# Performance work log

Hardware: AMD Instinct MI355X
Metric: run time of the kernel (lower is better)

The kernel has to match this reference:

```python
import jax, jax.numpy as jnp
import numpy as np

N, M, E, HID, H = 50000, 4000, 320000, 128, 2
EPS = 1e-5  # torch BatchNorm1d eps


def _lrelu(x):
    return jnp.where(x >= 0, x, 0.2 * x)


def _bn(x, g, b):
    # BatchNorm1d in training mode: biased batch statistics over dim 0
    m = x.mean(0)
    v = ((x - m) ** 2).mean(0)
    return g * (x - m) * jax.lax.rsqrt(v + EPS) + b


def _seg_softmax(a, idx, n):
    # softmax of a[E,heads] normalized per node index idx (PyG softmax)
    mx = jax.ops.segment_max(a, idx, num_segments=n)
    e = jnp.exp(a - mx[idx])
    s = jax.ops.segment_sum(e, idx, num_segments=n)
    return e / s[idx]


def _hgconv(x, he_n, he_e, he_w, W, att, bias, heads):
    # PyG HypergraphConv(use_attention=True, concat=False)
    xl = (x @ W).reshape(N, heads, HID)                  # lin(x) -> [N,heads,C]
    # hyperedge_attr = incidence^T @ x  (matches to_dense_adj path in HGAT)
    ea = jax.ops.segment_sum(x[he_n], he_e, num_segments=M)  # [M,F]
    eal = (ea @ W).reshape(M, heads, HID)                # lin(hyperedge_attr)
    a = (jnp.concatenate([xl[he_n], eal[he_e]], axis=-1) * att[0]).sum(-1)  # [E,heads]
    a = _seg_softmax(_lrelu(a), he_n, N)
    # degree normalizations
    Dn = jax.ops.segment_sum(he_w[he_e], he_n, num_segments=N)
    Dinv = jnp.where(Dn > 0, 1.0 / Dn, 0.0)
    Bn = jax.ops.segment_sum(jnp.ones((E,), x.dtype), he_e, num_segments=M)
    Binv = jnp.where(Bn > 0, 1.0 / Bn, 0.0)
    # node -> hyperedge
    m1 = Binv[he_e][:, None, None] * xl[he_n] * a[..., None]
    eo = jax.ops.segment_sum(m1, he_e, num_segments=M)   # [M,heads,C]
    # hyperedge -> node
    m2 = Dinv[he_n][:, None, None] * eo[he_e] * a[..., None]
    out = jax.ops.segment_sum(m2, he_n, num_segments=N)  # [N,heads,C]
    return out.mean(1) + bias                            # concat=False -> head mean


def _forward(x, he_w, lin1_w, lin1_b, bn1_g, bn1_b, h1_w, h1_att, h1_b,
             bn2_g, bn2_b, h2_w, h2_att, h2_b, bn3_g, bn3_b,
             lin2_w, lin2_b, bn4_g, bn4_b, he_n, he_e):
    src = x
    x = _bn(_lrelu(x @ lin1_w + lin1_b), bn1_g, bn1_b)
    x2 = _hgconv(x, he_n, he_e, he_w, h1_w, h1_att, h1_b, H)
    x = _bn(x + x2, bn2_g, bn2_b)
    x2 = _hgconv(x, he_n, he_e, he_w, h2_w, h2_att, h2_b, 1)
    x = _bn(x + x2, bn3_g, bn3_b)
    x = _lrelu(x @ lin2_w + lin2_b)
    return _bn(src + x, bn4_g, bn4_b)


def setup_inputs() -> dict:
    key = jax.random.key(0)
    ks = jax.random.split(key, 10)
    s = 0.05
    he_n = jax.random.randint(ks[0], (E,), 0, N, dtype=jnp.int32)
    he_e = (jnp.arange(E, dtype=jnp.int32) % M)  # every hyperedge id used
    return {
        'x': jax.random.normal(ks[1], (N, 128), jnp.float32),
        'he_n': he_n, 'he_e': he_e,
        'he_w': jnp.ones((M,), jnp.float32),
        'lin1_w': jax.random.normal(ks[2], (128, HID), jnp.float32) * s,
        'lin1_b': jnp.zeros((HID,), jnp.float32),
        'bn1_g': jnp.ones((HID,), jnp.float32), 'bn1_b': jnp.zeros((HID,), jnp.float32),
        'h1_w': jax.random.normal(ks[3], (HID, H * HID), jnp.float32) * s,
        'h1_att': jax.random.normal(ks[4], (1, H, 2 * HID), jnp.float32) * s,
        'h1_b': jnp.zeros((HID,), jnp.float32),
        'bn2_g': jnp.ones((HID,), jnp.float32), 'bn2_b': jnp.zeros((HID,), jnp.float32),
        'h2_w': jax.random.normal(ks[5], (HID, HID), jnp.float32) * s,
        'h2_att': jax.random.normal(ks[6], (1, 1, 2 * HID), jnp.float32) * s,
        'h2_b': jnp.zeros((HID,), jnp.float32),
        'bn3_g': jnp.ones((HID,), jnp.float32), 'bn3_b': jnp.zeros((HID,), jnp.float32),
        'lin2_w': jax.random.normal(ks[7], (HID, 128), jnp.float32) * s,
        'lin2_b': jnp.zeros((128,), jnp.float32),
        'bn4_g': jnp.ones((128,), jnp.float32), 'bn4_b': jnp.zeros((128,), jnp.float32),
    }


def reference(x, he_n, he_e, he_w, lin1_w, lin1_b, bn1_g, bn1_b, h1_w, h1_att, h1_b,
              bn2_g, bn2_b, h2_w, h2_att, h2_b, bn3_g, bn3_b,
              lin2_w, lin2_b, bn4_g, bn4_b):
    return _forward(x, he_w, lin1_w, lin1_b, bn1_g, bn1_b, h1_w, h1_att, h1_b,
                    bn2_g, bn2_b, h2_w, h2_att, h2_b, bn3_g, bn3_b,
                    lin2_w, lin2_b, bn4_g, bn4_b, he_n, he_e)
```

## Files before the change

### kernel.cpp

```cpp
#include <hip/hip_runtime.h>
#include <math.h>

constexpr int Nn = 50000;
constexpr int Mm = 4000;
constexpr int Ee = 320000;
constexpr int KPB = Ee / Mm;
constexpr float BINV = 1.0f / (float)KPB;
constexpr float EPSf = 1e-5f;
constexpr int NBKT = 16;
constexpr int NBSCAN = 49;

__device__ __forceinline__ float lrelu_f(float x) { return x >= 0.f ? x : 0.2f * x; }

__device__ __forceinline__ float wave_sum(float v) {
#pragma unroll
    for (int o = 32; o >= 1; o >>= 1) v += __shfl_xor(v, o, 64);
    return v;
}

__device__ __forceinline__ void finalize_to_lds(const float* __restrict__ st,
                                                const float* __restrict__ g,
                                                const float* __restrict__ b,
                                                float* ABsh, int t) {
    if (t < 128) {
        double ds = 0, dq = 0;
#pragma unroll
        for (int i = 0; i < NBKT; i++) {
            ds += (double)st[i * 256 + t];
            dq += (double)st[i * 256 + 128 + t];
        }
        double mean = ds / (double)Nn;
        double var = dq / (double)Nn - mean * mean;
        float rstd = (float)(1.0 / sqrt(var + (double)EPSf));
        float A = g[t] * rstd;
        ABsh[t] = A;
        ABsh[128 + t] = b[t] - (float)mean * A;
    }
    __syncthreads();
}

__device__ void scan_body(const int* __restrict__ counts, int* __restrict__ offs,
                          int b, int t) {
    __shared__ int sdi[256];
    int pre = 0;
    for (int i = t; i < b * 1024; i += 256) pre += counts[i];
    sdi[t] = pre;
    __syncthreads();
    for (int st = 128; st >= 1; st >>= 1) {
        if (t < st) sdi[t] += sdi[t + st];
        __syncthreads();
    }
    int run0 = sdi[0];
    __syncthreads();
    int c4[4];
    int s = 0;
#pragma unroll
    for (int i = 0; i < 4; i++) {
        int n = b * 1024 + t * 4 + i;
        c4[i] = (n < Nn) ? counts[n] : 0;
        s += c4[i];
    }
    sdi[t] = s;
    __syncthreads();
    for (int off = 1; off < 256; off <<= 1) {
        int v = (t >= off) ? sdi[t - off] : 0;
        __syncthreads();
        sdi[t] += v;
        __syncthreads();
    }
    int run = sdi[t] - s + run0;
#pragma unroll
    for (int i = 0; i < 4; i++) {
        int n = b * 1024 + t * 4 + i;
        if (n < Nn) offs[n] = run;
        run += c4[i];
    }
    if (b == NBSCAN - 1 && t == 255) offs[Nn] = run0 + sdi[255];
}

template <int ROWS, bool LRELU, bool PROBN, bool RESID, bool STATS, bool PACKH2, bool SCANX>
__global__ __launch_bounds__(256) void gemmT(const float* __restrict__ A, size_t aystride,
                                             const float* __restrict__ B, int ldb,
                                             const float* __restrict__ bias, float scale,
                                             const float* __restrict__ stIn,
                                             const float* __restrict__ fing,
                                             const float* __restrict__ finb,
                                             const float* __restrict__ resid,
                                             float* __restrict__ stF,
                                             float* __restrict__ C, int ldc, int R,
                                             int gemmBlocksX,
                                             const int* __restrict__ counts,
                                             int* __restrict__ offs) {
    constexpr int RPT = ROWS / 16;
    const int t = threadIdx.x;
    if (SCANX && (int)blockIdx.x >= gemmBlocksX) {
        if (blockIdx.y == 0) scan_body(counts, offs, blockIdx.x - gemmBlocksX, t);
        return;
    }
    __shared__ float As[16][ROWS + 4];
    __shared__ float Bs[16][128];
    __shared__ float Sred[STATS ? 16 : 1][STATS ? 128 : 1];
    __shared__ float ABsh[PROBN ? 256 : 1];
    const int ty = t >> 4, tx = t & 15;
    const int row0 = blockIdx.x * ROWS;
    const int bcol = blockIdx.y * 128;
    A += (size_t)blockIdx.y * aystride;

    if (PROBN) finalize_to_lds(stIn, fing, finb, ABsh, t);

    float4 acc[RPT][2];
#pragma unroll
    for (int i = 0; i < RPT; i++)
#pragma unroll
        for (int q = 0; q < 2; q++) acc[i][q] = make_float4(0.f, 0.f, 0.f, 0.f);

    for (int k0 = 0; k0 < 128; k0 += 16) {
        if (ROWS == 64) {
            int r = t >> 2, kc = (t & 3) * 4;
            int rr = row0 + r;
            rr = rr < R ? rr : R - 1;
            float4 av = *(const float4*)(A + (size_t)rr * 128 + k0 + kc);
            if (PROBN) {
                float4 sA = *(const float4*)&ABsh[k0 + kc];
                float4 sB = *(const float4*)&ABsh[128 + k0 + kc];
                av.x = av.x * sA.x + sB.x; av.y = av.y * sA.y + sB.y;
                av.z = av.z * sA.z + sB.z; av.w = av.w * sA.w + sB.w;
            }
            As[kc + 0][r] = av.x; As[kc + 1][r] = av.y;
            As[kc + 2][r] = av.z; As[kc + 3][r] = av.w;
        } else {
            int r = t >> 3, kc = (t & 7) * 2;
            int rr = row0 + r;
            rr = rr < R ? rr : R - 1;
            float2 av = *(const float2*)(A + (size_t)rr * 128 + k0 + kc);
            if (PROBN) {
                av.x = av.x * ABsh[k0 + kc] + ABsh[128 + k0 + kc];
                av.y = av.y * ABsh[k0 + kc + 1] + ABsh[128 + k0 + kc + 1];
            }
            As[kc + 0][r] = av.x;
            As[kc + 1][r] = av.y;
        }
        {
            int kk = t >> 5, c4 = (t & 31) * 4;
            float4 bv0 = *(const float4*)(B + (size_t)(k0 + kk) * ldb + bcol + c4);
            float4 bv1 = *(const float4*)(B + (size_t)(k0 + kk + 8) * ldb + bcol + c4);
            *(float4*)&Bs[kk][c4] = bv0;
            *(float4*)&Bs[kk + 8][c4] = bv1;
        }
        __syncthreads();
#pragma unroll
        for (int kk = 0; kk < 16; kk++) {
            float ar[RPT];
            if (RPT == 4) {
                float4 a4 = *(const float4*)&As[kk][ty * 4];
                ar[0] = a4.x; ar[1] = a4.y; ar[2] = a4.z; ar[3] = a4.w;
            } else {
                float2 a2 = *(const float2*)&As[kk][ty * 2];
                ar[0] = a2.x; ar[RPT - 1] = a2.y;
            }
            float4 b0 = *(const float4*)&Bs[kk][4 * tx];
            float4 b1 = *(const float4*)&Bs[kk][64 + 4 * tx];
#pragma unroll
            for (int i = 0; i < RPT; i++) {
                acc[i][0].x = fmaf(ar[i], b0.x, acc[i][0].x);
                acc[i][0].y = fmaf(ar[i], b0.y, acc[i][0].y);
                acc[i][0].z = fmaf(ar[i], b0.z, acc[i][0].z);
                acc[i][0].w = fmaf(ar[i], b0.w, acc[i][0].w);
                acc[i][1].x = fmaf(ar[i], b1.x, acc[i][1].x);
                acc[i][1].y = fmaf(ar[i], b1.y, acc[i][1].y);
                acc[i][1].z = fmaf(ar[i], b1.z, acc[i][1].z);
                acc[i][1].w = fmaf(ar[i], b1.w, acc[i][1].w);
            }
        }
        __syncthreads();
    }

    float4 bv0 = make_float4(0.f, 0.f, 0.f, 0.f), bv1 = bv0;
    if (bias) {
        bv0 = *(const float4*)(bias + bcol + 4 * tx);
        bv1 = *(const float4*)(bias + bcol + 64 + 4 * tx);
    }
    float4 cs0 = make_float4(0.f, 0.f, 0.f, 0.f), cs1 = cs0, cq0 = cs0, cq1 = cs0;
#pragma unroll
    for (int i = 0; i < RPT; i++) {
        int row = row0 + ty * RPT + i;
        if (row >= R) continue;
        float4 v0, v1;
        v0.x = acc[i][0].x * scale + bv0.x; v0.y = acc[i][0].y * scale + bv0.y;
        v0.z = acc[i][0].z * scale + bv0.z; v0.w = acc[i][0].w * scale + bv0.w;
        v1.x = acc[i][1].x * scale + bv1.x; v1.y = acc[i][1].y * scale + bv1.y;
        v1.z = acc[i][1].z * scale + bv1.z; v1.w = acc[i][1].w * scale + bv1.w;
        if (LRELU) {
            v0.x = lrelu_f(v0.x); v0.y = lrelu_f(v0.y); v0.z = lrelu_f(v0.z); v0.w = lrelu_f(v0.w);
            v1.x = lrelu_f(v1.x); v1.y = lrelu_f(v1.y); v1.z = lrelu_f(v1.z); v1.w = lrelu_f(v1.w);
        }
        if (RESID) {
            float4 r0 = *(const float4*)(resid + (size_t)row * 128 + bcol + 4 * tx);
            float4 r1 = *(const float4*)(resid + (size_t)row * 128 + bcol + 64 + 4 * tx);
            v0.x += r0.x; v0.y += r0.y; v0.z += r0.z; v0.w += r0.w;
            v1.x += r1.x; v1.y += r1.y; v1.z += r1.z; v1.w += r1.w;
        }
        if (PACKH2) {
            int h = blockIdx.y;
            float* c0 = C + (size_t)row * ldc + 8 * tx + 2 * h;
            *(float2*)(c0) = make_float2(v0.x, v0.y);
            *(float2*)(c0 + 4) = make_float2(v0.z, v0.w);
            float* c1 = C + (size_t)row * ldc + 128 + 8 * tx + 2 * h;
            *(float2*)(c1) = make_float2(v1.x, v1.y);
            *(float2*)(c1 + 4) = make_float2(v1.z, v1.w);
        } else {
            *(float4*)(C + (size_t)row * ldc + bcol + 4 * tx) = v0;
            *(float4*)(C + (size_t)row * ldc + bcol + 64 + 4 * tx) = v1;
        }
        if (STATS) {
            cs0.x += v0.x; cs0.y += v0.y; cs0.z += v0.z; cs0.w += v0.w;
            cs1.x += v1.x; cs1.y += v1.y; cs1.z += v1.z; cs1.w += v1.w;
            cq0.x += v0.x * v0.x; cq0.y += v0.y * v0.y; cq0.z += v0.z * v0.z; cq0.w += v0.w * v0.w;
            cq1.x += v1.x * v1.x; cq1.y += v1.y * v1.y; cq1.z += v1.z * v1.z; cq1.w += v1.w * v1.w;
        }
    }
    if (STATS) {
        int bkt = blockIdx.x & (NBKT - 1);
#pragma unroll
        for (int pass = 0; pass < 2; pass++) {
            *(float4*)&Sred[ty][4 * tx] = pass ? cq0 : cs0;
            *(float4*)&Sred[ty][64 + 4 * tx] = pass ? cq1 : cs1;
            __syncthreads();
            if (t < 128) {
                float tot = 0.f;
#pragma unroll
                for (int r = 0; r < 16; r++) tot += Sred[r][t];
                atomicAdd(&stF[bkt * 256 + pass * 128 + t], tot);
            }
            __syncthreads();
        }
    }
}

__global__ void count_edges_watt(const int* __restrict__ he_n, int* __restrict__ counts,
                                 const float* __restrict__ h1_w, const float* __restrict__ h1_att,
                                 const float* __restrict__ h2_w, const float* __restrict__ h2_att,
                                 float* __restrict__ wnA, float* __restrict__ weA,
                                 int* __restrict__ he_nT) {
    int t = threadIdx.x;
    if (blockIdx.x == 1250) {
        for (int j = 0; j < 3; j++) {
            int id = t + 256 * j;
            if (id >= 768) break;
            int which = id / 384;
            int rem = id % 384;
            int h3 = rem >> 7, k = rem & 127;
            float s = 0.f;
            if (h3 < 2) {
                const float* wrow = h1_w + (size_t)k * 256 + h3 * 128;
                const float* arow = h1_att + h3 * 256 + which * 128;
                for (int c = 0; c < 128; c++) s += wrow[c] * arow[c];
            } else {
                const float* wrow = h2_w + (size_t)k * 128;
                const float* arow = h2_att + which * 128;
                for (int c = 0; c < 128; c++) s += wrow[c] * arow[c];
            }
            (which ? weA : wnA)[h3 * 128 + k] = s;
        }
        return;
    }
    int g = blockIdx.x * 256 + t;
    if (g < Ee) {
        int m = g / KPB;
        int k = g - m * KPB;
        int n = he_n[m + (size_t)k * Mm];
        he_nT[g] = n;
        atomicAdd(&counts[n], 1);
    }
}

template <int H, bool FILL>
__global__ __launch_bounds__(256) void bn_dots(const float* __restrict__ X,
                                               const float* __restrict__ stIn,
                                               const float* __restrict__ fing,
                                               const float* __restrict__ finb,
                                               float* __restrict__ ABout,
                                               const float* __restrict__ wn,
                                               const float* __restrict__ we,
                                               float* __restrict__ an,
                                               float* __restrict__ pe,
                                               const int* __restrict__ he_n,
                                               const int* __restrict__ offs,
                                               int* __restrict__ cursor,
                                               int* __restrict__ eid, int mainBlocks) {
    int t = threadIdx.x;
    if (FILL && (int)blockIdx.x >= mainBlocks) {
        int e = (blockIdx.x - mainBlocks) * 256 + t;
        if (e < Ee) {
            int n = he_n[e];
            int p = atomicAdd(&cursor[n], 1);
            eid[offs[n] + p] = e;
        }
        return;
    }
    __shared__ float ABsh[256];
    finalize_to_lds(stIn, fing, finb, ABsh, t);
    if (blockIdx.x == 0) ABout[t] = ABsh[t];
    int w = t >> 6, lane = t & 63;
    float a0 = ABsh[lane], a1 = ABsh[lane + 64];
    float b0 = ABsh[128 + lane], b1 = ABsh[192 + lane];
    float wn0[H], wn1[H], we0[H], we1[H];
#pragma unroll
    for (int h = 0; h < H; h++) {
        wn0[h] = wn[h * 128 + lane]; wn1[h] = wn[h * 128 + 64 + lane];
        we0[h] = we[h * 128 + lane]; we1[h] = we[h * 128 + 64 + lane];
    }
#pragma unroll
    for (int nn = 0; nn < 4; nn++) {
        int row = blockIdx.x * 16 + w * 4 + nn;
        const float* xr = X + (size_t)row * 128;
        float v0 = xr[lane] * a0 + b0;
        float v1 = xr[lane + 64] * a1 + b1;
        float pv[H], qv[H];
#pragma unroll
        for (int h = 0; h < H; h++) {
            pv[h] = wave_sum(v0 * wn0[h] + v1 * wn1[h]);
            qv[h] = wave_sum(v0 * we0[h] + v1 * we1[h]);
        }
        if (lane == 0) {
            if (H == 2) {
                *(float2*)&an[row * 2] = make_float2(pv[0], pv[1]);
                *(float2*)&pe[row * 2] = make_float2(qv[0], qv[1]);
            } else {
                an[row] = pv[0];
                pe[row] = qv[0];
            }
        }
    }
}

__global__ __launch_bounds__(256) void bn_out(const float* __restrict__ X,
                                              const float* __restrict__ stIn,
                                              const float* __restrict__ fing,
                                              const float* __restrict__ finb,
                                              float* __restrict__ Y) {
    __shared__ float ABsh[256];
    int t = threadIdx.x;
    finalize_to_lds(stIn, fing, finb, ABsh, t);
    int w = t >> 6, lane = t & 63;
    float a0 = ABsh[lane], a1 = ABsh[lane + 64];
    float b0 = ABsh[128 + lane], b1 = ABsh[192 + lane];
#pragma unroll
    for (int nn = 0; nn < 4; nn++) {
        int row = blockIdx.x * 16 + w * 4 + nn;
        const float* xr = X + (size_t)row * 128;
        float* yr = Y + (size_t)row * 128;
        yr[lane] = xr[lane] * a0 + b0;
        yr[lane + 64] = xr[lane + 64] * a1 + b1;
    }
}

template <int H>
__global__ __launch_bounds__(256) void ea_from_pe(const int* __restrict__ he_nT,
                                                  const float* __restrict__ pe,
                                                  float* __restrict__ ae) {
    int w = threadIdx.x >> 6, lane = threadIdx.x & 63;
    int m = blockIdx.x * 4 + w;
    if (m >= Mm) return;
    float s[H];
#pragma unroll
    for (int h = 0; h < H; h++) s[h] = 0.f;
    for (int k = lane; k < KPB; k += 64) {
        int idx = he_nT[m * KPB + k];
        if (H == 2) {
            float2 p2 = *(const float2*)(pe + (size_t)idx * 2);
            s[0] += p2.x;
            s[H - 1] += p2.y;
        } else {
            s[0] += pe[idx];
        }
    }
#pragma unroll
    for (int h = 0; h < H; h++) s[h] = wave_sum(s[h]);
    if (lane == 0)
#pragma unroll
        for (int h = 0; h < H; h++) ae[m * H + h] = s[h];
}

template <int H>
__global__ __launch_bounds__(256) void seg_softmax(const int* __restrict__ offs,
                                                   const int* __restrict__ eid,
                                                   const float* __restrict__ an,
                                                   const float* __restrict__ ae,
                                                   const float* __restrict__ he_w,
                                                   float* __restrict__ nsp) {
    int t = threadIdx.x;
    int wv = t >> 6, lane = t & 63;
    int q = lane >> 3, li = lane & 7;
    int n = blockIdx.x * 32 + wv * 8 + q;
    bool valid = n < Nn;
    int base = valid ? offs[n] : 0;
    int deg = valid ? offs[n + 1] - base : 0;
    float anv[H];
#pragma unroll
    for (int h = 0; h < H; h++) anv[h] = valid ? an[n * H + h] : 0.f;

    bool h0 = li < deg, h1 = li + 8 < deg;
    int m0 = 0, m1 = 0;
    float l0[H], l1[H];
    float mx[H];
#pragma unroll
    for (int h = 0; h < H; h++) { mx[h] = -INFINITY; l0[h] = 0.f; l1[h] = 0.f; }
    if (h0) {
        m0 = eid[base + li] % Mm;
#pragma unroll
        for (int h = 0; h < H; h++) {
            l0[h] = lrelu_f(anv[h] + ae[m0 * H + h]);
            mx[h] = fmaxf(mx[h], l0[h]);
        }
    }
    if (h1) {
        m1 = eid[base + li + 8] % Mm;
#pragma unroll
        for (int h = 0; h < H; h++) {
            l1[h] = lrelu_f(anv[h] + ae[m1 * H + h]);
            mx[h] = fmaxf(mx[h], l1[h]);
        }
    }
    for (int c = li + 16; c < deg; c += 8) {
        int m = eid[base + c] % Mm;
#pragma unroll
        for (int h = 0; h < H; h++) mx[h] = fmaxf(mx[h], lrelu_f(anv[h] + ae[m * H + h]));
    }
#pragma unroll
    for (int h = 0; h < H; h++) {
#pragma unroll
        for (int o = 1; o <= 4; o <<= 1) mx[h] = fmaxf(mx[h], __shfl_xor(mx[h], o, 64));
    }
    float sm[H];
#pragma unroll
    for (int h = 0; h < H; h++) sm[h] = 0.f;
    float dn = 0.f;
    if (h0) {
        dn += he_w[m0];
#pragma unroll
        for (int h = 0; h < H; h++) sm[h] += expf(l0[h] - mx[h]);
    }
    if (h1) {
        dn += he_w[m1];
#pragma unroll
        for (int h = 0; h < H; h++) sm[h] += expf(l1[h] - mx[h]);
    }
    for (int c = li + 16; c < deg; c += 8) {
        int m = eid[base + c] % Mm;
        dn += he_w[m];
#pragma unroll
        for (int h = 0; h < H; h++) sm[h] += expf(lrelu_f(anv[h] + ae[m * H + h]) - mx[h]);
    }
#pragma unroll
    for (int o = 1; o <= 4; o <<= 1) dn += __shfl_xor(dn, o, 64);
#pragma unroll
    for (int h = 0; h < H; h++) {
#pragma unroll
        for (int o = 1; o <= 4; o <<= 1) sm[h] += __shfl_xor(sm[h], o, 64);
    }
    if (valid && li == 0) {
        float Dv = dn > 0.f ? 1.0f / dn : 0.0f;
        if (H == 2) {
            *(float4*)(nsp + (size_t)n * 8) = make_float4(anv[0], anv[H - 1], mx[0], mx[H - 1]);
            *(float4*)(nsp + (size_t)n * 8 + 4) =
                make_float4(1.f / sm[0], 1.f / sm[H - 1], 0.5f * Dv, 0.f);
        } else {
            *(float4*)(nsp + (size_t)n * 4) = make_float4(anv[0], mx[0], 1.f / sm[0], Dv);
        }
    }
}

template <int H>
__global__ __launch_bounds__(256) void s_build(const float* __restrict__ X,
                                               const float* __restrict__ AB,
                                               const int* __restrict__ he_nT,
                                               const float* __restrict__ nsp,
                                               const float* __restrict__ ae,
                                               float* __restrict__ S) {
    __shared__ int idx[KPB];
    __shared__ float av[KPB][H];
    __shared__ float red[8][H][128];
    int m = blockIdx.x, t = threadIdx.x;
    int g = t >> 5, l = t & 31;
    if (t < KPB) {
        int nd = he_nT[m * KPB + t];
        idx[t] = nd;
        if (H == 2) {
            float4 pa = *(const float4*)(nsp + (size_t)nd * 8);
            float4 pb = *(const float4*)(nsp + (size_t)nd * 8 + 4);
            float2 a2 = *(const float2*)(ae + (size_t)m * 2);
            av[t][0] = expf(lrelu_f(pa.x + a2.x) - pa.z) * pb.x;
            av[t][H - 1] = expf(lrelu_f(pa.y + a2.y) - pa.w) * pb.y;
        } else {
            float4 pa = *(const float4*)(nsp + (size_t)nd * 4);
            float aem = ae[m];
            av[t][0] = expf(lrelu_f(pa.x + aem) - pa.y) * pa.z;
        }
    }
    __syncthreads();
    float4 A4 = ((const float4*)AB)[l];
    float4 B4 = ((const float4*)(AB + 128))[l];
    float4 acc[H];
#pragma unroll
    for (int h = 0; h < H; h++) acc[h] = make_float4(0.f, 0.f, 0.f, 0.f);
#pragma unroll
    for (int kk = 0; kk < KPB / 8; kk++) {
        int k = g + kk * 8;
        float4 v = ((const float4*)(X + (size_t)idx[k] * 128))[l];
        v.x = v.x * A4.x + B4.x;
        v.y = v.y * A4.y + B4.y;
        v.z = v.z * A4.z + B4.z;
        v.w = v.w * A4.w + B4.w;
#pragma unroll
        for (int h = 0; h < H; h++) {
            float a = av[k][h];
            acc[h].x = fmaf(a, v.x, acc[h].x);
            acc[h].y = fmaf(a, v.y, acc[h].y);
            acc[h].z = fmaf(a, v.z, acc[h].z);
            acc[h].w = fmaf(a, v.w, acc[h].w);
        }
    }
#pragma unroll
    for (int h = 0; h < H; h++) *(float4*)&red[g][h][l * 4] = acc[h];
    __syncthreads();
    if (t < 32 * H) {
        int h = t >> 5, l2 = t & 31;
        float4 s = make_float4(0.f, 0.f, 0.f, 0.f);
#pragma unroll
        for (int gg = 0; gg < 8; gg++) {
            float4 r = *(const float4*)&red[gg][h][l2 * 4];
            s.x += r.x; s.y += r.y; s.z += r.z; s.w += r.w;
        }
        ((float4*)(S + ((size_t)h * Mm + m) * 128))[l2] = s;
    }
}

template <int H>
__global__ __launch_bounds__(256) void node_agg(const int* __restrict__ offs,
                                                const int* __restrict__ eid,
                                                const float* __restrict__ nsp,
                                                const float* __restrict__ ae,
                                                const float* __restrict__ eo,
                                                const float* __restrict__ bias,
                                                const float* __restrict__ AB,
                                                float* __restrict__ stF,
                                                float* __restrict__ T) {
    __shared__ float smem[4][256];
    __shared__ float redS[4][128], redQ[4][128];
    int t = threadIdx.x;
    int w = t >> 6, lane = t & 63;
    int n0 = blockIdx.x * 16 + w * 4;
    int o = offs[n0 + (lane < 4 ? lane : 4)];
    int b0 = __shfl(o, 0, 64);
    int b1 = __shfl(o, 1, 64);
    int b2 = __shfl(o, 2, 64);
    int b3 = __shfl(o, 3, 64);
    int b4 = __shfl(o, 4, 64);
    int cnt = b4 - b0;
    int cnt64 = cnt < 64 ? cnt : 64;

    if (lane < cnt64) {
        int slot = b0 + lane;
        int j = (slot >= b1) + (slot >= b2) + (slot >= b3);
        int e = eid[slot];
        int m = e % Mm;
        if (H == 2) {
            float4 pa = *(const float4*)(nsp + (size_t)(n0 + j) * 8);
            float4 pb = *(const float4*)(nsp + (size_t)(n0 + j) * 8 + 4);
            float2 a2 = *(const float2*)(ae + (size_t)m * 2);
            float c0 = expf(lrelu_f(pa.x + a2.x) - pa.z) * pb.x * pb.z;
            float c1 = expf(lrelu_f(pa.y + a2.y) - pa.w) * pb.y * pb.z;
            *(float4*)&smem[w][4 * lane] = make_float4(__int_as_float(m), c0, c1, 0.f);
        } else {
            float4 pa = *(const float4*)(nsp + (size_t)(n0 + j) * 4);
            float c = expf(lrelu_f(pa.x + ae[m]) - pa.y) * pa.z * pa.w;
            *(float2*)&smem[w][2 * lane] = make_float2(__int_as_float(m), c);
        }
    }
    __syncthreads();

    int s1 = min(b1 - b0, cnt64), s2 = min(b2 - b0, cnt64), s3 = min(b3 - b0, cnt64);
    float2 acc0 = make_float2(0.f, 0.f), acc1 = acc0, acc2 = acc0, acc3 = acc0;

#define NA_BODY(ACC, CBEG, CEND)                                                \
    {                                                                           \
        int c = (CBEG);                                                         \
        for (; c + 1 < (CEND); c += 2) {                                        \
            if (H == 2) {                                                       \
                float4 sa = *(const float4*)&smem[w][4 * c];                    \
                float4 sb = *(const float4*)&smem[w][4 * (c + 1)];              \
                float4 ea = *(const float4*)(eo + (size_t)__float_as_int(sa.x) * 256 + 4 * lane); \
                float4 eb = *(const float4*)(eo + (size_t)__float_as_int(sb.x) * 256 + 4 * lane); \
                ACC.x += sa.y * ea.x + sa.z * ea.z + sb.y * eb.x + sb.z * eb.z; \
                ACC.y += sa.y * ea.y + sa.z * ea.w + sb.y * eb.y + sb.z * eb.w; \
            } else {                                                            \
                float2 sa = *(const float2*)&smem[w][2 * c];                    \
                float2 sb = *(const float2*)&smem[w][2 * (c + 1)];              \
                float2 ea = *(const float2*)(eo + (size_t)__float_as_int(sa.x) * 128 + 2 * lane); \
                float2 eb = *(const float2*)(eo + (size_t)__float_as_int(sb.x) * 128 + 2 * lane); \
                ACC.x += sa.y * ea.x + sb.y * eb.x;                             \
                ACC.y += sa.y * ea.y + sb.y * eb.y;                             \
            }                                                                   \
        }                                                                       \
        if (c < (CEND)) {                                                       \
            if (H == 2) {                                                       \
                float4 sa = *(const float4*)&smem[w][4 * c];                    \
                float4 ea = *(const float4*)(eo + (size_t)__float_as_int(sa.x) * 256 + 4 * lane); \
                ACC.x += sa.y * ea.x + sa.z * ea.z;                             \
                ACC.y += sa.y * ea.y + sa.z * ea.w;                             \
            } else {                                                            \
                float2 sa = *(const float2*)&smem[w][2 * c];                    \
                float2 ea = *(const float2*)(eo + (size_t)__float_as_int(sa.x) * 128 + 2 * lane); \
                ACC.x += sa.y * ea.x;                                           \
                ACC.y += sa.y * ea.y;                                           \
            }                                                                   \
        }                                                                       \
    }
    NA_BODY(acc0, 0, s1)
    NA_BODY(acc1, s1, s2)
    NA_BODY(acc2, s2, s3)
    NA_BODY(acc3, s3, cnt64)
#undef NA_BODY

    for (int ss = 64; ss < cnt; ss++) {
        int slot = b0 + ss;
        int j = (slot >= b1) + (slot >= b2) + (slot >= b3);
        int e = eid[slot];
        int m = e % Mm;
        float cx, cy;
        if (H == 2) {
            float4 pa = *(const float4*)(nsp + (size_t)(n0 + j) * 8);
            float4 pb = *(const float4*)(nsp + (size_t)(n0 + j) * 8 + 4);
            float2 a2 = *(const float2*)(ae + (size_t)m * 2);
            float c0 = expf(lrelu_f(pa.x + a2.x) - pa.z) * pb.x * pb.z;
            float c1 = expf(lrelu_f(pa.y + a2.y) - pa.w) * pb.y * pb.z;
            float4 ev = *(const float4*)(eo + (size_t)m * 256 + 4 * lane);
            cx = c0 * ev.x + c1 * ev.z;
            cy = c0 * ev.y + c1 * ev.w;
        } else {
            float4 pa = *(const float4*)(nsp + (size_t)(n0 + j) * 4);
            float c = expf(lrelu_f(pa.x + ae[m]) - pa.y) * pa.z * pa.w;
            float2 ev = *(const float2*)(eo + (size_t)m * 128 + 2 * lane);
            cx = c * ev.x;
            cy = c * ev.y;
        }
        if (j == 0) { acc0.x += cx; acc0.y += cy; }
        else if (j == 1) { acc1.x += cx; acc1.y += cy; }
        else if (j == 2) { acc2.x += cx; acc2.y += cy; }
        else { acc3.x += cx; acc3.y += cy; }
    }

    int col = 2 * lane;
    float2 A2 = *(const float2*)(AB + col);
    float2 B2 = *(const float2*)(AB + 128 + col);
    float2 bi = *(const float2*)(bias + col);
    float cs0 = 0.f, cs1 = 0.f, cq0 = 0.f, cq1 = 0.f;
    float2 accs[4] = {acc0, acc1, acc2, acc3};
#pragma unroll
    for (int j = 0; j < 4; j++) {
        int n = n0 + j;
        float2 xr = *(const float2*)(T + (size_t)n * 128 + col);
        float r0 = xr.x * A2.x + B2.x + bi.x + accs[j].x;
        float r1 = xr.y * A2.y + B2.y + bi.y + accs[j].y;
        *(float2*)(T + (size_t)n * 128 + col) = make_float2(r0, r1);
        cs0 += r0; cs1 += r1;
        cq0 += r0 * r0; cq1 += r1 * r1;
    }
    redS[w][col] = cs0; redS[w][col + 1] = cs1;
    redQ[w][col] = cq0; redQ[w][col + 1] = cq1;
    __syncthreads();
    if (t < 128) {
        float s = 0.f, qq = 0.f;
#pragma unroll
        for (int ww = 0; ww < 4; ww++) { s += redS[ww][t]; qq += redQ[ww][t]; }
        int bkt = blockIdx.x & (NBKT - 1);
        atomicAdd(&stF[bkt * 256 + t], s);
        atomicAdd(&stF[bkt * 256 + 128 + t], qq);
    }
}

extern "C" void kernel_launch(void* const* d_in, const int* in_sizes, int n_in,
                              void* d_out, int out_size, void* d_ws, size_t ws_size,
                              hipStream_t stream) {
    const float* x = (const float*)d_in[0];
    const int* he_n = (const int*)d_in[1];
    const float* he_w = (const float*)d_in[3];
    const float* lin1_w = (const float*)d_in[4];
    const float* lin1_b = (const float*)d_in[5];
    const float* bn1_g = (const float*)d_in[6];
    const float* bn1_b = (const float*)d_in[7];
    const float* h1_w = (const float*)d_in[8];
    const float* h1_att = (const float*)d_in[9];
    const float* h1_b = (const float*)d_in[10];
    const float* bn2_g = (const float*)d_in[11];
    const float* bn2_b = (const float*)d_in[12];
    const float* h2_w = (const float*)d_in[13];
    const float* h2_att = (const float*)d_in[14];
    const float* h2_b = (const float*)d_in[15];
    const float* bn3_g = (const float*)d_in[16];
    const float* bn3_b = (const float*)d_in[17];
    const float* lin2_w = (const float*)d_in[18];
    const float* lin2_b = (const float*)d_in[19];
    const float* bn4_g = (const float*)d_in[20];
    const float* bn4_b = (const float*)d_in[21];
    float* out = (float*)d_out;

    char* ws = (char*)d_ws;
    size_t off = 0;
    auto alloc = [&](size_t bytes) -> char* {
        char* p = ws + off;
        off = (off + bytes + 255) & ~(size_t)255;
        return p;
    };
    int* counts = (int*)alloc((size_t)Nn * 4);
    int* cursor = (int*)alloc((size_t)Nn * 4);
    float* stats = (float*)alloc((size_t)4 * NBKT * 256 * 4);
    size_t zbytes = off;
    int* offs = (int*)alloc((size_t)(Nn + 1) * 4);
    int* eid = (int*)alloc((size_t)Ee * 4);
    int* he_nT = (int*)alloc((size_t)Ee * 4);
    float* an = (float*)alloc((size_t)Nn * 2 * 4);
    float* pe = (float*)alloc((size_t)Nn * 2 * 4);
    float* ae = (float*)alloc((size_t)Mm * 2 * 4);
    float* nsp = (float*)alloc((size_t)Nn * 8 * 4);
    float* S = (float*)alloc((size_t)2 * Mm * 128 * 4);
    float* eo = (float*)alloc((size_t)2 * Mm * 128 * 4);
    float* wnA = (float*)alloc(384 * 4);
    float* weA = (float*)alloc(384 * 4);
    float* AB = (float*)alloc(2 * 256 * 4);
    float* buf = (float*)alloc((size_t)Nn * 128 * 4);

    float* st0 = stats;
    float* st1 = stats + NBKT * 256;
    float* st2 = stats + 2 * NBKT * 256;
    float* st3 = stats + 3 * NBKT * 256;
    float *AB1 = AB, *AB2 = AB + 256;

    hipMemsetAsync(d_ws, 0, zbytes, stream);

    constexpr int GB32 = (Nn + 31) / 32;
    count_edges_watt<<<1251, 256, 0, stream>>>(he_n, counts, h1_w, h1_att, h2_w, h2_att,
                                               wnA, weA, he_nT);

    gemmT<32, true, false, false, true, false, true><<<dim3(GB32 + NBSCAN, 1), 256, 0, stream>>>(
        x, 0, lin1_w, 128, lin1_b, 1.f, nullptr, nullptr, nullptr, nullptr, st0, buf, 128, Nn,
        GB32, counts, offs);
    bn_dots<2, true><<<3125 + 1250, 256, 0, stream>>>(buf, st0, bn1_g, bn1_b, AB1, wnA, weA,
                                                      an, pe, he_n, offs, cursor, eid, 3125);

    ea_from_pe<2><<<Mm / 4, 256, 0, stream>>>(he_nT, pe, ae);
    seg_softmax<2><<<(Nn + 31) / 32, 256, 0, stream>>>(offs, eid, an, ae, he_w, nsp);
    s_build<2><<<Mm, 256, 0, stream>>>(buf, AB1, he_nT, nsp, ae, S);
    gemmT<32, false, false, false, false, true, false><<<dim3(125, 2), 256, 0, stream>>>(
        S, (size_t)Mm * 128, h1_w, 256, nullptr, BINV, nullptr, nullptr, nullptr, nullptr,
        nullptr, eo, 256, Mm, 125, nullptr, nullptr);
    node_agg<2><<<3125, 256, 0, stream>>>(offs, eid, nsp, ae, eo, h1_b, AB1, st1, buf);

    bn_dots<1, false><<<3125, 256, 0, stream>>>(buf, st1, bn2_g, bn2_b, AB2, wnA + 256,
                                                weA + 256, an, pe, nullptr, nullptr, nullptr,
                                                nullptr, 3125);

    ea_from_pe<1><<<Mm / 4, 256, 0, stream>>>(he_nT, pe, ae);
    seg_softmax<1><<<(Nn + 31) / 32, 256, 0, stream>>>(offs, eid, an, ae, he_w, nsp);
    s_build<1><<<Mm, 256, 0, stream>>>(buf, AB2, he_nT, nsp, ae, S);
    gemmT<32, false, false, false, false, false, false><<<dim3(125, 1), 256, 0, stream>>>(
        S, 0, h2_w, 128, nullptr, BINV, nullptr, nullptr, nullptr, nullptr, nullptr,
        eo, 128, Mm, 125, nullptr, nullptr);
    node_agg<1><<<3125, 256, 0, stream>>>(offs, eid, nsp, ae, eo, h2_b, AB2, st2, buf);

    gemmT<32, true, true, true, true, false, false><<<dim3(GB32, 1), 256, 0, stream>>>(
        buf, 0, lin2_w, 128, lin2_b, 1.f, st2, bn3_g, bn3_b, x, st3, buf, 128, Nn,
        GB32, nullptr, nullptr);
    bn_out<<<3125, 256, 0, stream>>>(buf, st3, bn4_g, bn4_b, out);
}
```

Before: 394.0 us.

## Add single-stage full-K GEMM kernel for node-level linear layers

Adds a gemmB kernel for the two N-row linear layers. It loads the whole 128x128 weight matrix and a 32x128 A tile into one 80KB LDS pool, then runs the full K loop with no per-k-slice barriers. The existing gemmT is reduced to the plain variant used by the hyperedge GEMMs. This removes the 8 load/sync rounds per block, but the large LDS footprint limits blocks per CU, so latency hiding drops and every block must reload the full weight matrix.

Result: slower. 417.3 us (+5.9%).

```diff
diff --git a/kernel.cpp b/kernel.cpp
--- a/kernel.cpp
+++ b/kernel.cpp
@@ -40,8 +40,7 @@
 }
 
 __device__ void scan_body(const int* __restrict__ counts, int* __restrict__ offs,
-                          int b, int t) {
-    __shared__ int sdi[256];
+                          int b, int t, int* sdi) {
     int pre = 0;
     for (int i = t; i < b * 1024; i += 256) pre += counts[i];
     sdi[t] = pre;
@@ -78,36 +77,159 @@
     if (b == NBSCAN - 1 && t == 255) offs[Nn] = run0 + sdi[255];
 }
 
-template <int ROWS, bool LRELU, bool PROBN, bool RESID, bool STATS, bool PACKH2, bool SCANX>
-__global__ __launch_bounds__(256) void gemmT(const float* __restrict__ A, size_t aystride,
-                                             const float* __restrict__ B, int ldb,
-                                             const float* __restrict__ bias, float scale,
+template <bool LRELU, bool PROBN, bool RESID, bool STATS, bool SCANX>
+__global__ __launch_bounds__(256) void gemmB(const float* __restrict__ A,
+                                             const float* __restrict__ B,
+                                             const float* __restrict__ bias,
                                              const float* __restrict__ stIn,
                                              const float* __restrict__ fing,
                                              const float* __restrict__ finb,
                                              const float* __restrict__ resid,
                                              float* __restrict__ stF,
-                                             float* __restrict__ C, int ldc, int R,
+                                             float* __restrict__ C, int R,
                                              int gemmBlocksX,
                                              const int* __restrict__ counts,
                                              int* __restrict__ offs) {
+    __shared__ float pool[20480];
+    const int t = threadIdx.x;
+    if (SCANX && (int)blockIdx.x >= gemmBlocksX) {
+        scan_body(counts, offs, blockIdx.x - gemmBlocksX, t, (int*)pool);
+        return;
+    }
+    const int ty = t >> 4, tx = t & 15;
+    const int row0 = blockIdx.x * 32;
+    const int rA = t & 31, kA = (t >> 5) * 16;
+
+    float Areg[16], Breg[16];
+    if (PROBN) {
+        finalize_to_lds(stIn, fing, finb, pool, t);
+#pragma unroll
+        for (int j = 0; j < 16; j++) {
+            Areg[j] = pool[kA + j];
+            Breg[j] = pool[128 + kA + j];
+        }
+        __syncthreads();
+    }
+
+    {
+        const int cB = (t & 31) * 4, kB0 = (t >> 5) * 16;
+#pragma unroll
+        for (int j = 0; j < 16; j++) {
+            float4 bv = *(const float4*)(B + (size_t)(kB0 + j) * 128 + cB);
+            *(float4*)&pool[4096 + (kB0 + j) * 128 + cB] = bv;
+        }
+    }
+    {
+        int rr = row0 + rA;
+        rr = rr < R ? rr : R - 1;
+        const float* Ar = A + (size_t)rr * 128 + kA;
+#pragma unroll
+        for (int p = 0; p < 4; p++) {
+            float4 av = *(const float4*)(Ar + 4 * p);
+            float vv[4] = {av.x, av.y, av.z, av.w};
+#pragma unroll
+            for (int q = 0; q < 4; q++) {
+                float v = vv[q];
+                if (PROBN) v = v * Areg[4 * p + q] + Breg[4 * p + q];
+                pool[(kA + 4 * p + q) * 32 + rA] = v;
+            }
+        }
+    }
+    __syncthreads();
+
+    float4 acc[2][2];
+#pragma unroll
+    for (int i = 0; i < 2; i++)
+#pragma unroll
+        for (int q = 0; q < 2; q++) acc[i][q] = make_float4(0.f, 0.f, 0.f, 0.f);
+
+#pragma unroll 8
+    for (int kk = 0; kk < 128; kk++) {
+        float2 a2 = *(const float2*)&pool[kk * 32 + ty * 2];
+        float4 b0 = *(const float4*)&pool[4096 + kk * 128 + 4 * tx];
+        float4 b1 = *(const float4*)&pool[4096 + kk * 128 + 64 + 4 * tx];
+        float ar[2] = {a2.x, a2.y};
+#pragma unroll
+        for (int i = 0; i < 2; i++) {
+            acc[i][0].x = fmaf(ar[i], b0.x, acc[i][0].x);
+            acc[i][0].y = fmaf(ar[i], b0.y, acc[i][0].y);
+            acc[i][0].z = fmaf(ar[i], b0.z, acc[i][0].z);
+            acc[i][0].w = fmaf(ar[i], b0.w, acc[i][0].w);
+            acc[i][1].x = fmaf(ar[i], b1.x, acc[i][1].x);
+            acc[i][1].y = fmaf(ar[i], b1.y, acc[i][1].y);
+            acc[i][1].z = fmaf(ar[i], b1.z, acc[i][1].z);
+            acc[i][1].w = fmaf(ar[i], b1.w, acc[i][1].w);
+        }
+    }
+
+    float4 bv0 = make_float4(0.f, 0.f, 0.f, 0.f), bv1 = bv0;
+    if (bias) {
+        bv0 = *(const float4*)(bias + 4 * tx);
+        bv1 = *(const float4*)(bias + 64 + 4 * tx);
+    }
+    float4 cs0 = make_float4(0.f, 0.f, 0.f, 0.f), cs1 = cs0, cq0 = cs0, cq1 = cs0;
+#pragma unroll
+    for (int i = 0; i < 2; i++) {
+        int row = row0 + ty * 2 + i;
+        if (row >= R) continue;
+        float4 v0, v1;
+        v0.x = acc[i][0].x + bv0.x; v0.y = acc[i][0].y + bv0.y;
+        v0.z = acc[i][0].z + bv0.z; v0.w = acc[i][0].w + bv0.w;
+        v1.x = acc[i][1].x + bv1.x; v1.y = acc[i][1].y + bv1.y;
+        v1.z = acc[i][1].z + bv1.z; v1.w = acc[i][1].w + bv1.w;
+        if (LRELU) {
+            v0.x = lrelu_f(v0.x); v0.y = lrelu_f(v0.y); v0.z = lrelu_f(v0.z); v0.w = lrelu_f(v0.w);
+            v1.x = lrelu_f(v1.x); v1.y = lrelu_f(v1.y); v1.z = lrelu_f(v1.z); v1.w = lrelu_f(v1.w);
+        }
+        if (RESID) {
+            float4 r0 = *(const float4*)(resid + (size_t)row * 128 + 4 * tx);
+            float4 r1 = *(const float4*)(resid + (size_t)row * 128 + 64 + 4 * tx);
+            v0.x += r0.x; v0.y += r0.y; v0.z += r0.z; v0.w += r0.w;
+            v1.x += r1.x; v1.y += r1.y; v1.z += r1.z; v1.w += r1.w;
+        }
+        *(float4*)(C + (size_t)row * 128 + 4 * tx) = v0;
+        *(float4*)(C + (size_t)row * 128 + 64 + 4 * tx) = v1;
+        if (STATS) {
+            cs0.x += v0.x; cs0.y += v0.y; cs0.z += v0.z; cs0.w += v0.w;
+            cs1.x += v1.x; cs1.y += v1.y; cs1.z += v1.z; cs1.w += v1.w;
+            cq0.x += v0.x * v0.x; cq0.y += v0.y * v0.y; cq0.z += v0.z * v0.z; cq0.w += v0.w * v0.w;
+            cq1.x += v1.x * v1.x; cq1.y += v1.y * v1.y; cq1.z += v1.z * v1.z; cq1.w += v1.w * v1.w;
+        }
+    }
+    if (STATS) {
+        __syncthreads();
+        float (*Sred)[128] = (float(*)[128])pool;
+        int bkt = blockIdx.x & (NBKT - 1);
+#pragma unroll
+        for (int pass = 0; pass < 2; pass++) {
+            *(float4*)&Sred[ty][4 * tx] = pass ? cq0 : cs0;
+            *(float4*)&Sred[ty][64 + 4 * tx] = pass ? cq1 : cs1;
+            __syncthreads();
+            if (t < 128) {
+                float tot = 0.f;
+#pragma unroll
+                for (int r = 0; r < 16; r++) tot += Sred[r][t];
+                atomicAdd(&stF[bkt * 256 + pass * 128 + t], tot);
+            }
+            __syncthreads();
+        }
+    }
+}
+
+template <int ROWS, bool PACKH2>
+__global__ __launch_bounds__(256) void gemmT(const float* __restrict__ A, size_t aystride,
+                                             const float* __restrict__ B, int ldb,
+                                             float scale,
+                                             float* __restrict__ C, int ldc, int R) {
     constexpr int RPT = ROWS / 16;
     const int t = threadIdx.x;
-    if (SCANX && (int)blockIdx.x >= gemmBlocksX) {
-        if (blockIdx.y == 0) scan_body(counts, offs, blockIdx.x - gemmBlocksX, t);
-        return;
-    }
     __shared__ float As[16][ROWS + 4];
     __shared__ float Bs[16][128];
-    __shared__ float Sred[STATS ? 16 : 1][STATS ? 128 : 1];
-    __shared__ float ABsh[PROBN ? 256 : 1];
     const int ty = t >> 4, tx = t & 15;
     const int row0 = blockIdx.x * ROWS;
     const int bcol = blockIdx.y * 128;
     A += (size_t)blockIdx.y * aystride;
 
-    if (PROBN) finalize_to_lds(stIn, fing, finb, ABsh, t);
-
     float4 acc[RPT][2];
 #pragma unroll
     for (int i = 0; i < RPT; i++)
@@ -115,28 +237,11 @@
         for (int q = 0; q < 2; q++) acc[i][q] = make_float4(0.f, 0.f, 0.f, 0.f);
 
     for (int k0 = 0; k0 < 128; k0 += 16) {
-        if (ROWS == 64) {
-            int r = t >> 2, kc = (t & 3) * 4;
-            int rr = row0 + r;
-            rr = rr < R ? rr : R - 1;
-            float4 av = *(const float4*)(A + (size_t)rr * 128 + k0 + kc);
-            if (PROBN) {
-                float4 sA = *(const float4*)&ABsh[k0 + kc];
-                float4 sB = *(const float4*)&ABsh[128 + k0 + kc];
-                av.x = av.x * sA.x + sB.x; av.y = av.y * sA.y + sB.y;
-                av.z = av.z * sA.z + sB.z; av.w = av.w * sA.w + sB.w;
-            }
-            As[kc + 0][r] = av.x; As[kc + 1][r] = av.y;
-            As[kc + 2][r] = av.z; As[kc + 3][r] = av.w;
-        } else {
+        {
             int r = t >> 3, kc = (t & 7) * 2;
             int rr = row0 + r;
             rr = rr < R ? rr : R - 1;
             float2 av = *(const float2*)(A + (size_t)rr * 128 + k0 + kc);
-            if (PROBN) {
-                av.x = av.x * ABsh[k0 + kc] + ABsh[128 + k0 + kc];
-                av.y = av.y * ABsh[k0 + kc + 1] + ABsh[128 + k0 + kc + 1];
-            }
             As[kc + 0][r] = av.x;
             As[kc + 1][r] = av.y;
         }
@@ -151,10 +256,7 @@
 #pragma unroll
         for (int kk = 0; kk < 16; kk++) {
             float ar[RPT];
-            if (RPT == 4) {
-                float4 a4 = *(const float4*)&As[kk][ty * 4];
-                ar[0] = a4.x; ar[1] = a4.y; ar[2] = a4.z; ar[3] = a4.w;
-            } else {
+            {
                 float2 a2 = *(const float2*)&As[kk][ty * 2];
                 ar[0] = a2.x; ar[RPT - 1] = a2.y;
             }
@@ -175,31 +277,15 @@
         __syncthreads();
     }
 
-    float4 bv0 = make_float4(0.f, 0.f, 0.f, 0.f), bv1 = bv0;
-    if (bias) {
-        bv0 = *(const float4*)(bias + bcol + 4 * tx);
-        bv1 = *(const float4*)(bias + bcol + 64 + 4 * tx);
-    }
-    float4 cs0 = make_float4(0.f, 0.f, 0.f, 0.f), cs1 = cs0, cq0 = cs0, cq1 = cs0;
 #pragma unroll
     for (int i = 0; i < RPT; i++) {
         int row = row0 + ty * RPT + i;
         if (row >= R) continue;
         float4 v0, v1;
-        v0.x = acc[i][0].x * scale + bv0.x; v0.y = acc[i][0].y * scale + bv0.y;
-        v0.z = acc[i][0].z * scale + bv0.z; v0.w = acc[i][0].w * scale + bv0.w;
-        v1.x = acc[i][1].x * scale + bv1.x; v1.y = acc[i][1].y * scale + bv1.y;
-        v1.z = acc[i][1].z * scale + bv1.z; v1.w = acc[i][1].w * scale + bv1.w;
-        if (LRELU) {
-            v0.x = lrelu_f(v0.x); v0.y = lrelu_f(v0.y); v0.z = lrelu_f(v0.z); v0.w = lrelu_f(v0.w);
-            v1.x = lrelu_f(v1.x); v1.y = lrelu_f(v1.y); v1.z = lrelu_f(v1.z); v1.w = lrelu_f(v1.w);
-        }
-        if (RESID) {
-            float4 r0 = *(const float4*)(resid + (size_t)row * 128 + bcol + 4 * tx);
-            float4 r1 = *(const float4*)(resid + (size_t)row * 128 + bcol + 64 + 4 * tx);
-            v0.x += r0.x; v0.y += r0.y; v0.z += r0.z; v0.w += r0.w;
-            v1.x += r1.x; v1.y += r1.y; v1.z += r1.z; v1.w += r1.w;
-        }
+        v0.x = acc[i][0].x * scale; v0.y = acc[i][0].y * scale;
+        v0.z = acc[i][0].z * scale; v0.w = acc[i][0].w * scale;
+        v1.x = acc[i][1].x * scale; v1.y = acc[i][1].y * scale;
+        v1.z = acc[i][1].z * scale; v1.w = acc[i][1].w * scale;
         if (PACKH2) {
             int h = blockIdx.y;
             float* c0 = C + (size_t)row * ldc + 8 * tx + 2 * h;
@@ -211,28 +297,6 @@
         } else {
             *(float4*)(C + (size_t)row * ldc + bcol + 4 * tx) = v0;
             *(float4*)(C + (size_t)row * ldc + bcol + 64 + 4 * tx) = v1;
-        }
-        if (STATS) {
-            cs0.x += v0.x; cs0.y += v0.y; cs0.z += v0.z; cs0.w += v0.w;
-            cs1.x += v1.x; cs1.y += v1.y; cs1.z += v1.z; cs1.w += v1.w;
-            cq0.x += v0.x * v0.x; cq0.y += v0.y * v0.y; cq0.z += v0.z * v0.z; cq0.w += v0.w * v0.w;
-            cq1.x += v1.x * v1.x; cq1.y += v1.y * v1.y; cq1.z += v1.z * v1.z; cq1.w += v1.w * v1.w;
-        }
-    }
-    if (STATS) {
-        int bkt = blockIdx.x & (NBKT - 1);
-#pragma unroll
-        for (int pass = 0; pass < 2; pass++) {
-            *(float4*)&Sred[ty][4 * tx] = pass ? cq0 : cs0;
-            *(float4*)&Sred[ty][64 + 4 * tx] = pass ? cq1 : cs1;
-            __syncthreads();
-            if (t < 128) {
-                float tot = 0.f;
-#pragma unroll
-                for (int r = 0; r < 16; r++) tot += Sred[r][t];
-                atomicAdd(&stF[bkt * 256 + pass * 128 + t], tot);
-            }
-            __syncthreads();
         }
     }
 }
@@ -743,8 +807,8 @@
     count_edges_watt<<<1251, 256, 0, stream>>>(he_n, counts, h1_w, h1_att, h2_w, h2_att,
                                                wnA, weA, he_nT);
 
-    gemmT<32, true, false, false, true, false, true><<<dim3(GB32 + NBSCAN, 1), 256, 0, stream>>>(
-        x, 0, lin1_w, 128, lin1_b, 1.f, nullptr, nullptr, nullptr, nullptr, st0, buf, 128, Nn,
+    gemmB<true, false, false, true, true><<<GB32 + NBSCAN, 256, 0, stream>>>(
+        x, lin1_w, lin1_b, nullptr, nullptr, nullptr, nullptr, st0, buf, Nn,
         GB32, counts, offs);
     bn_dots<2, true><<<3125 + 1250, 256, 0, stream>>>(buf, st0, bn1_g, bn1_b, AB1, wnA, weA,
                                                       an, pe, he_n, offs, cursor, eid, 3125);
@@ -752,9 +816,8 @@
     ea_from_pe<2><<<Mm / 4, 256, 0, stream>>>(he_nT, pe, ae);
     seg_softmax<2><<<(Nn + 31) / 32, 256, 0, stream>>>(offs, eid, an, ae, he_w, nsp);
     s_build<2><<<Mm, 256, 0, stream>>>(buf, AB1, he_nT, nsp, ae, S);
-    gemmT<32, false, false, false, false, true, false><<<dim3(125, 2), 256, 0, stream>>>(
-        S, (size_t)Mm * 128, h1_w, 256, nullptr, BINV, nullptr, nullptr, nullptr, nullptr,
-        nullptr, eo, 256, Mm, 125, nullptr, nullptr);
+    gemmT<32, true><<<dim3(125, 2), 256, 0, stream>>>(
+        S, (size_t)Mm * 128, h1_w, 256, BINV, eo, 256, Mm);
     node_agg<2><<<3125, 256, 0, stream>>>(offs, eid, nsp, ae, eo, h1_b, AB1, st1, buf);
 
     bn_dots<1, false><<<3125, 256, 0, stream>>>(buf, st1, bn2_g, bn2_b, AB2, wnA + 256,
@@ -764,13 +827,12 @@
     ea_from_pe<1><<<Mm / 4, 256, 0, stream>>>(he_nT, pe, ae);
     seg_softmax<1><<<(Nn + 31) / 32, 256, 0, stream>>>(offs, eid, an, ae, he_w, nsp);
     s_build<1><<<Mm, 256, 0, stream>>>(buf, AB2, he_nT, nsp, ae, S);
-    gemmT<32, false, false, false, false, false, false><<<dim3(125, 1), 256, 0, stream>>>(
-        S, 0, h2_w, 128, nullptr, BINV, nullptr, nullptr, nullptr, nullptr, nullptr,
-        eo, 128, Mm, 125, nullptr, nullptr);
+    gemmT<32, false><<<dim3(125, 1), 256, 0, stream>>>(
+        S, 0, h2_w, 128, BINV, eo, 128, Mm);
     node_agg<1><<<3125, 256, 0, stream>>>(offs, eid, nsp, ae, eo, h2_b, AB2, st2, buf);
 
-    gemmT<32, true, true, true, true, false, false><<<dim3(GB32, 1), 256, 0, stream>>>(
-        buf, 0, lin2_w, 128, lin2_b, 1.f, st2, bn3_g, bn3_b, x, st3, buf, 128, Nn,
+    gemmB<true, true, true, true, false><<<GB32, 256, 0, stream>>>(
+        buf, lin2_w, lin2_b, st2, bn3_g, bn3_b, x, st3, buf, Nn,
         GB32, nullptr, nullptr);
     bn_out<<<3125, 256, 0, stream>>>(buf, st3, bn4_g, bn4_b, out);
 }
```
